# Kernel optimization log

Hardware: AMD Instinct MI355X
Metric: run time of the kernel (lower is better)

## Reference

```python
import jax, jax.numpy as jnp
import numpy as np
from jax import lax

VOCAB, NUM_CLASSES = 21128, 53
EMB, FILT, K = 128, 128, 3
B, L = 512, 512


def setup_inputs() -> dict:
    key = jax.random.key(0)
    ks = jax.random.split(key, 8)
    char_ids = jax.random.randint(ks[0], (B, L), 0, VOCAB, dtype=jnp.int64 if jax.config.jax_enable_x64 else jnp.int32)
    pos_e1 = jax.random.randint(ks[1], (B,), 0, L - 1, dtype=jnp.int32)
    pos_e2 = jax.random.randint(ks[2], (B,), 0, L - 1, dtype=jnp.int32)
    emb_table = jax.random.normal(ks[3], (VOCAB, EMB), dtype=jnp.float32) * 0.02
    emb_table = emb_table.at[0].set(0.0)  # padding_idx=0
    conv_w = jax.random.normal(ks[4], (FILT, EMB, K), dtype=jnp.float32) * (1.0 / np.sqrt(EMB * K))
    conv_b = jax.random.normal(ks[5], (FILT,), dtype=jnp.float32) * 0.01
    fc_w = jax.random.normal(ks[6], (NUM_CLASSES, FILT * 3), dtype=jnp.float32) * (1.0 / np.sqrt(FILT * 3))
    fc_b = jax.random.normal(ks[7], (NUM_CLASSES,), dtype=jnp.float32) * 0.01
    return {"char_ids": char_ids, "pos_e1": pos_e1, "pos_e2": pos_e2,
            "emb_table": emb_table, "conv_w": conv_w, "conv_b": conv_b,
            "fc_w": fc_w, "fc_b": fc_b}


def reference(char_ids, pos_e1, pos_e2, emb_table, conv_w, conv_b, fc_w, fc_b):
    b, seq = char_ids.shape
    x = emb_table[char_ids]                      # (b, L, E)
    x = jnp.transpose(x, (0, 2, 1))              # (b, E, L)
    conv_out = lax.conv_general_dilated(
        x, conv_w, window_strides=(1,), padding=[(K // 2, K // 2)],
        dimension_numbers=("NCH", "OIH", "NCH"))
    conv_out = jax.nn.relu(conv_out + conv_b[None, :, None])  # (b, F, L)

    # sort + clip entity boundaries, replicate e1==e2 -> e2=e1+1 adjustment
    e1 = jnp.clip(jnp.minimum(pos_e1, pos_e2), 0, seq)
    e2 = jnp.clip(jnp.maximum(pos_e1, pos_e2), 0, seq)
    e2 = jnp.where(e1 == e2, jnp.minimum(e1 + 1, seq), e2)

    idx = jnp.arange(seq)[None, :]               # (1, L)
    m1 = idx < jnp.maximum(e1, 1)[:, None]       # [:e1] or [:1] if e1==0
    m2 = (idx >= e1[:, None]) & (idx < e2[:, None])
    m3 = idx >= jnp.minimum(e2, seq - 1)[:, None]  # [e2:] or last col if e2==L

    neg = jnp.float32(-jnp.inf)
    def seg_max(mask):
        return jnp.max(jnp.where(mask[:, None, :], conv_out, neg), axis=-1)  # (b, F)

    pooled = jnp.concatenate([seg_max(m1), seg_max(m2), seg_max(m3)], axis=-1)  # (b, 3F)
    return pooled @ fc_w.T + fc_b
```

## Files before the change

kernel.cpp:

```cpp
#include <hip/hip_runtime.h>
#include <stdint.h>

#define VOCAB 21128
#define NUMC  53
#define EMB   128
#define SEQ   512
#define BATCH 512

typedef __bf16 bf16x8 __attribute__((ext_vector_type(8)));
typedef float f32x4 __attribute__((ext_vector_type(4)));

__device__ __forceinline__ unsigned int f2bf1(float f) {
    union { float f; unsigned int u; } v; v.f = f;
    return (v.u + 0x7FFFu + ((v.u >> 16) & 1u)) >> 16;
}
__device__ __forceinline__ unsigned int pack2(float a, float b) {
    return f2bf1(a) | (f2bf1(b) << 16);
}

__global__ void prep_kernel(const float* __restrict__ emb, const float* __restrict__ cw,
                            unsigned short* __restrict__ Tb, unsigned short* __restrict__ Wp) {
    int idx = blockIdx.x * blockDim.x + threadIdx.x;
    const int n8 = VOCAB * EMB / 8;
    if (idx < n8) {
        const float4* src = (const float4*)emb + (size_t)idx * 2;
        float4 a = src[0], b = src[1];
        uint4 o;
        o.x = pack2(a.x, a.y);
        o.y = pack2(a.z, a.w);
        o.z = pack2(b.x, b.y);
        o.w = pack2(b.z, b.w);
        *(uint4*)(Tb + (size_t)idx * 8) = o;
    }
    if (idx < 12 * 8 * 64 * 8) {
        int j = idx & 7, l = (idx >> 3) & 63, g = (idx >> 9) & 7, s = idx >> 12;
        int kk = s * 32 + (l >> 4) * 8 + j;
        int f = g * 16 + (l & 15);
        int tap = kk >> 7, e = kk & 127;
        Wp[idx] = (unsigned short)f2bf1(cw[(f * EMB + e) * 3 + tap]);
    }
}

__launch_bounds__(512, 2)
__global__ void pcnn_tile(const int* __restrict__ cid, const int* __restrict__ p1,
                          const int* __restrict__ p2,
                          const unsigned short* __restrict__ Tb,
                          const unsigned short* __restrict__ Wp,
                          float* __restrict__ Pd) {
    __shared__ __align__(16) unsigned short xs[130 * 136];
    __shared__ float pstage[2][3][128];

    const int bx   = blockIdx.x;
    const int b    = bx >> 2;
    const int tq   = bx & 3;
    const int tid  = threadIdx.x;
    const int lane = tid & 63;
    const int w    = tid >> 6;
    const int wm   = w & 1;
    const int wn   = w >> 1;
    const int quad = lane >> 4;
    const int lc   = lane & 15;

    const char* TbB = (const char*)Tb;
    const int cc = tid & 15;
    const int r0 = tid >> 4;
    int ids[5];
#pragma unroll
    for (int i = 0; i < 5; ++i) {
        int r = r0 + 32 * i;
        int p = tq * 128 + r - 1;
        ids[i] = (r < 130 && p >= 0 && p < SEQ) ? cid[(size_t)b * SEQ + p] : 0;
    }
    uint4 g[5];
#pragma unroll
    for (int i = 0; i < 5; ++i) {
        int r = r0 + 32 * i;
        if (r < 130) g[i] = *(const uint4*)(TbB + (size_t)(unsigned)ids[i] * 256u + cc * 16);
    }
#pragma unroll
    for (int i = 0; i < 5; ++i) {
        int r = r0 + 32 * i;
        if (r < 130) *(uint4*)(&xs[r * 136 + cc * 8]) = g[i];
    }

    int e1 = min(p1[b], p2[b]);
    int e2 = max(p1[b], p2[b]);
    if (e1 == e2) e2 = min(e1 + 1, SEQ);
    const int e1m = max(e1, 1);

    __syncthreads();

    f32x4 acc[4][2];
#pragma unroll
    for (int mt = 0; mt < 4; ++mt)
#pragma unroll
        for (int nt = 0; nt < 2; ++nt)
            acc[mt][nt] = (f32x4){0.f, 0.f, 0.f, 0.f};

#pragma unroll
    for (int s = 0; s < 12; ++s) {
        const int tap = s >> 2;
        const int eb  = (s & 3) * 32;
        bf16x8 b0 = *(const bf16x8*)(Wp + (size_t)((s * 8 + wn * 2) * 64 + lane) * 8);
        bf16x8 b1 = *(const bf16x8*)(Wp + (size_t)((s * 8 + wn * 2 + 1) * 64 + lane) * 8);
        bf16x8 af[4];
#pragma unroll
        for (int mt = 0; mt < 4; ++mt) {
            int r = wm * 64 + mt * 16 + lc + tap;
            af[mt] = *(const bf16x8*)(xs + r * 136 + eb + quad * 8);
        }
#pragma unroll
        for (int mt = 0; mt < 4; ++mt) {
            acc[mt][0] = __builtin_amdgcn_mfma_f32_16x16x32_bf16(af[mt], b0, acc[mt][0], 0, 0, 0);
            acc[mt][1] = __builtin_amdgcn_mfma_f32_16x16x32_bf16(af[mt], b1, acc[mt][1], 0, 0, 0);
        }
    }

    float smax[3][2];
#pragma unroll
    for (int s3 = 0; s3 < 3; ++s3) { smax[s3][0] = -1e30f; smax[s3][1] = -1e30f; }
#pragma unroll
    for (int mt = 0; mt < 4; ++mt)
#pragma unroll
        for (int reg = 0; reg < 4; ++reg) {
            int p = tq * 128 + wm * 64 + mt * 16 + quad * 4 + reg;
            float a0 = (p < e1m) ? 0.f : -2e30f;
            float a1 = (p >= e1 && p < e2) ? 0.f : -2e30f;
            float a2 = (p >= e2) ? 0.f : -2e30f;
#pragma unroll
            for (int nt = 0; nt < 2; ++nt) {
                float v = acc[mt][nt][reg];
                smax[0][nt] = fmaxf(smax[0][nt], v + a0);
                smax[1][nt] = fmaxf(smax[1][nt], v + a1);
                smax[2][nt] = fmaxf(smax[2][nt], v + a2);
            }
        }

#pragma unroll
    for (int s3 = 0; s3 < 3; ++s3)
#pragma unroll
        for (int nt = 0; nt < 2; ++nt) {
            float v = smax[s3][nt];
            v = fmaxf(v, __shfl_xor(v, 16));
            v = fmaxf(v, __shfl_xor(v, 32));
            smax[s3][nt] = v;
        }
    if (lane < 16) {
#pragma unroll
        for (int s3 = 0; s3 < 3; ++s3)
#pragma unroll
            for (int nt = 0; nt < 2; ++nt)
                pstage[wm][s3][(wn * 2 + nt) * 16 + lc] = smax[s3][nt];
    }
    __syncthreads();

    if (tid < 384) {
        int s3 = tid >> 7, f = tid & 127;
        Pd[((size_t)b * 4 + tq) * 384 + tid] = fmaxf(pstage[0][s3][f], pstage[1][s3][f]);
    }
}

__launch_bounds__(256, 4)
__global__ void pcnn_combine(const float* __restrict__ Pd, const float* __restrict__ cb,
                             const float* __restrict__ fcw, const float* __restrict__ fcb,
                             float* __restrict__ out) {
    __shared__ float pooled[384];
    __shared__ float fcred[NUMC][4];
    const int b = blockIdx.x;
    const int tid = threadIdx.x;

    for (int j = tid; j < 384; j += 256) {
        const float* pp = Pd + (size_t)b * 4 * 384 + j;
        float m = fmaxf(fmaxf(pp[0], pp[384]), fmaxf(pp[768], pp[1152]));
        pooled[j] = fmaxf(m + cb[j & 127], 0.f);
    }
    __syncthreads();

    if (tid < 212) {
        int c = tid >> 2, q = tid & 3;
        const float* wrow = fcw + (size_t)c * 384 + q * 96;
        const float* pp   = pooled + q * 96;
        float sum = 0.f;
#pragma unroll 8
        for (int i = 0; i < 96; ++i) sum += wrow[i] * pp[i];
        fcred[c][q] = sum;
    }
    __syncthreads();
    if (tid < NUMC)
        out[(size_t)b * NUMC + tid] =
            fcred[tid][0] + fcred[tid][1] + fcred[tid][2] + fcred[tid][3] + fcb[tid];
}

extern "C" void kernel_launch(void* const* d_in, const int* in_sizes, int n_in,
                              void* d_out, int out_size, void* d_ws, size_t ws_size,
                              hipStream_t stream) {
    const int*   cid = (const int*)d_in[0];
    const int*   p1  = (const int*)d_in[1];
    const int*   p2  = (const int*)d_in[2];
    const float* emb = (const float*)d_in[3];
    const float* cw  = (const float*)d_in[4];
    const float* cb  = (const float*)d_in[5];
    const float* fcw = (const float*)d_in[6];
    const float* fcb = (const float*)d_in[7];
    float* out = (float*)d_out;

    unsigned short* Tb = (unsigned short*)d_ws;
    unsigned short* Wp = (unsigned short*)((char*)d_ws + (size_t)VOCAB * EMB * 2);
    float*          Pd = (float*)((char*)d_ws + (size_t)VOCAB * EMB * 2 + 98304);

    const int n8 = VOCAB * EMB / 8;
    const int prep_threads = 256;
    const int prep_blocks  = (n8 + prep_threads - 1) / prep_threads;
    prep_kernel<<<prep_blocks, prep_threads, 0, stream>>>(emb, cw, Tb, Wp);
    pcnn_tile<<<BATCH * 4, 512, 0, stream>>>(cid, p1, p2, Tb, Wp, Pd);
    pcnn_combine<<<BATCH, 256, 0, stream>>>(Pd, cb, fcw, fcb, out);
}
```

Before: 130.7 us.

## Gather fp32 embeddings directly in tile kernel and shrink tiles to 64 rows

Drops the full-vocabulary bf16 conversion pass. The tile kernel now gathers fp32 embedding rows for its tokens and converts them to bf16 in registers while staging into LDS. The tile shrinks to 64 sequence positions with 128 threads (two waves, each covering 64 filters), and each wave writes its partial maxima straight to the workspace, removing the LDS staging and the second barrier. The combine kernel now reduces 8 partials per segment instead of 4. In exchange, gathers read twice as many bytes, halo rows are duplicated across more tiles, and each block issues fewer parallel loads.

```diff
diff --git a/kernel.cpp b/kernel.cpp
--- a/kernel.cpp
+++ b/kernel.cpp
@@ -18,20 +18,8 @@
     return f2bf1(a) | (f2bf1(b) << 16);
 }
 
-__global__ void prep_kernel(const float* __restrict__ emb, const float* __restrict__ cw,
-                            unsigned short* __restrict__ Tb, unsigned short* __restrict__ Wp) {
+__global__ void prep_w(const float* __restrict__ cw, unsigned short* __restrict__ Wp) {
     int idx = blockIdx.x * blockDim.x + threadIdx.x;
-    const int n8 = VOCAB * EMB / 8;
-    if (idx < n8) {
-        const float4* src = (const float4*)emb + (size_t)idx * 2;
-        float4 a = src[0], b = src[1];
-        uint4 o;
-        o.x = pack2(a.x, a.y);
-        o.y = pack2(a.z, a.w);
-        o.z = pack2(b.x, b.y);
-        o.w = pack2(b.z, b.w);
-        *(uint4*)(Tb + (size_t)idx * 8) = o;
-    }
     if (idx < 12 * 8 * 64 * 8) {
         int j = idx & 7, l = (idx >> 3) & 63, g = (idx >> 9) & 7, s = idx >> 12;
         int kk = s * 32 + (l >> 4) * 8 + j;
@@ -41,46 +29,38 @@
     }
 }
 
-__launch_bounds__(512, 2)
+__launch_bounds__(128)
 __global__ void pcnn_tile(const int* __restrict__ cid, const int* __restrict__ p1,
-                          const int* __restrict__ p2,
-                          const unsigned short* __restrict__ Tb,
+                          const int* __restrict__ p2, const float* __restrict__ emb,
                           const unsigned short* __restrict__ Wp,
                           float* __restrict__ Pd) {
-    __shared__ __align__(16) unsigned short xs[130 * 136];
-    __shared__ float pstage[2][3][128];
+    __shared__ __align__(16) unsigned short xs[66 * 136];
 
     const int bx   = blockIdx.x;
-    const int b    = bx >> 2;
-    const int tq   = bx & 3;
+    const int b    = bx >> 3;
+    const int tq   = bx & 7;
     const int tid  = threadIdx.x;
     const int lane = tid & 63;
-    const int w    = tid >> 6;
-    const int wm   = w & 1;
-    const int wn   = w >> 1;
+    const int wn   = tid >> 6;
     const int quad = lane >> 4;
     const int lc   = lane & 15;
 
-    const char* TbB = (const char*)Tb;
-    const int cc = tid & 15;
-    const int r0 = tid >> 4;
-    int ids[5];
 #pragma unroll
-    for (int i = 0; i < 5; ++i) {
-        int r = r0 + 32 * i;
-        int p = tq * 128 + r - 1;
-        ids[i] = (r < 130 && p >= 0 && p < SEQ) ? cid[(size_t)b * SEQ + p] : 0;
-    }
-    uint4 g[5];
-#pragma unroll
-    for (int i = 0; i < 5; ++i) {
-        int r = r0 + 32 * i;
-        if (r < 130) g[i] = *(const uint4*)(TbB + (size_t)(unsigned)ids[i] * 256u + cc * 16);
-    }
-#pragma unroll
-    for (int i = 0; i < 5; ++i) {
-        int r = r0 + 32 * i;
-        if (r < 130) *(uint4*)(&xs[r * 136 + cc * 8]) = g[i];
+    for (int i = 0; i < 9; ++i) {
+        int task = tid + 128 * i;
+        if (task < 1056) {
+            int r = task >> 4, c = task & 15;
+            int p = tq * 64 + r - 1;
+            int id = (p >= 0 && p < SEQ) ? cid[(size_t)b * SEQ + p] : 0;
+            const float4* src = (const float4*)(emb + (size_t)id * EMB + c * 8);
+            float4 a = src[0], d = src[1];
+            uint4 o;
+            o.x = pack2(a.x, a.y);
+            o.y = pack2(a.z, a.w);
+            o.z = pack2(d.x, d.y);
+            o.w = pack2(d.z, d.w);
+            *(uint4*)(&xs[r * 136 + c * 8]) = o;
+        }
     }
 
     int e1 = min(p1[b], p2[b]);
@@ -90,45 +70,49 @@
 
     __syncthreads();
 
-    f32x4 acc[4][2];
+    f32x4 acc[4][4];
 #pragma unroll
     for (int mt = 0; mt < 4; ++mt)
 #pragma unroll
-        for (int nt = 0; nt < 2; ++nt)
+        for (int nt = 0; nt < 4; ++nt)
             acc[mt][nt] = (f32x4){0.f, 0.f, 0.f, 0.f};
 
 #pragma unroll
     for (int s = 0; s < 12; ++s) {
         const int tap = s >> 2;
         const int eb  = (s & 3) * 32;
-        bf16x8 b0 = *(const bf16x8*)(Wp + (size_t)((s * 8 + wn * 2) * 64 + lane) * 8);
-        bf16x8 b1 = *(const bf16x8*)(Wp + (size_t)((s * 8 + wn * 2 + 1) * 64 + lane) * 8);
         bf16x8 af[4];
 #pragma unroll
         for (int mt = 0; mt < 4; ++mt) {
-            int r = wm * 64 + mt * 16 + lc + tap;
+            int r = mt * 16 + lc + tap;
             af[mt] = *(const bf16x8*)(xs + r * 136 + eb + quad * 8);
         }
 #pragma unroll
-        for (int mt = 0; mt < 4; ++mt) {
-            acc[mt][0] = __builtin_amdgcn_mfma_f32_16x16x32_bf16(af[mt], b0, acc[mt][0], 0, 0, 0);
-            acc[mt][1] = __builtin_amdgcn_mfma_f32_16x16x32_bf16(af[mt], b1, acc[mt][1], 0, 0, 0);
+        for (int nt = 0; nt < 4; ++nt) {
+            int g = wn * 4 + nt;
+            bf16x8 bf = *(const bf16x8*)(Wp + (size_t)((s * 8 + g) * 64 + lane) * 8);
+#pragma unroll
+            for (int mt = 0; mt < 4; ++mt)
+                acc[mt][nt] = __builtin_amdgcn_mfma_f32_16x16x32_bf16(af[mt], bf, acc[mt][nt], 0, 0, 0);
         }
     }
 
-    float smax[3][2];
+    float smax[3][4];
 #pragma unroll
-    for (int s3 = 0; s3 < 3; ++s3) { smax[s3][0] = -1e30f; smax[s3][1] = -1e30f; }
+    for (int s3 = 0; s3 < 3; ++s3)
+#pragma unroll
+        for (int nt = 0; nt < 4; ++nt) smax[s3][nt] = -1e30f;
+
 #pragma unroll
     for (int mt = 0; mt < 4; ++mt)
 #pragma unroll
         for (int reg = 0; reg < 4; ++reg) {
-            int p = tq * 128 + wm * 64 + mt * 16 + quad * 4 + reg;
+            int p = tq * 64 + mt * 16 + quad * 4 + reg;
             float a0 = (p < e1m) ? 0.f : -2e30f;
             float a1 = (p >= e1 && p < e2) ? 0.f : -2e30f;
             float a2 = (p >= e2) ? 0.f : -2e30f;
 #pragma unroll
-            for (int nt = 0; nt < 2; ++nt) {
+            for (int nt = 0; nt < 4; ++nt) {
                 float v = acc[mt][nt][reg];
                 smax[0][nt] = fmaxf(smax[0][nt], v + a0);
                 smax[1][nt] = fmaxf(smax[1][nt], v + a1);
@@ -139,24 +123,19 @@
 #pragma unroll
     for (int s3 = 0; s3 < 3; ++s3)
 #pragma unroll
-        for (int nt = 0; nt < 2; ++nt) {
+        for (int nt = 0; nt < 4; ++nt) {
             float v = smax[s3][nt];
             v = fmaxf(v, __shfl_xor(v, 16));
             v = fmaxf(v, __shfl_xor(v, 32));
             smax[s3][nt] = v;
         }
     if (lane < 16) {
+        size_t base = ((size_t)(b * 8 + tq) * 3) * 128;
 #pragma unroll
         for (int s3 = 0; s3 < 3; ++s3)
 #pragma unroll
-            for (int nt = 0; nt < 2; ++nt)
-                pstage[wm][s3][(wn * 2 + nt) * 16 + lc] = smax[s3][nt];
-    }
-    __syncthreads();
-
-    if (tid < 384) {
-        int s3 = tid >> 7, f = tid & 127;
-        Pd[((size_t)b * 4 + tq) * 384 + tid] = fmaxf(pstage[0][s3][f], pstage[1][s3][f]);
+            for (int nt = 0; nt < 4; ++nt)
+                Pd[base + (size_t)s3 * 128 + wn * 64 + nt * 16 + lc] = smax[s3][nt];
     }
 }
 
@@ -170,9 +149,12 @@
     const int tid = threadIdx.x;
 
     for (int j = tid; j < 384; j += 256) {
-        const float* pp = Pd + (size_t)b * 4 * 384 + j;
-        float m = fmaxf(fmaxf(pp[0], pp[384]), fmaxf(pp[768], pp[1152]));
-        pooled[j] = fmaxf(m + cb[j & 127], 0.f);
+        int s3 = j >> 7, f = j & 127;
+        const float* pp = Pd + ((size_t)b * 8 * 3 + s3) * 128 + f;
+        float m = -1e30f;
+#pragma unroll
+        for (int tq = 0; tq < 8; ++tq) m = fmaxf(m, pp[(size_t)tq * 384]);
+        pooled[j] = fmaxf(m + cb[f], 0.f);
     }
     __syncthreads();
 
@@ -204,14 +186,10 @@
     const float* fcb = (const float*)d_in[7];
     float* out = (float*)d_out;
 
-    unsigned short* Tb = (unsigned short*)d_ws;
-    unsigned short* Wp = (unsigned short*)((char*)d_ws + (size_t)VOCAB * EMB * 2);
-    float*          Pd = (float*)((char*)d_ws + (size_t)VOCAB * EMB * 2 + 98304);
+    unsigned short* Wp = (unsigned short*)d_ws;
+    float*          Pd = (float*)((char*)d_ws + 98304);
 
-    const int n8 = VOCAB * EMB / 8;
-    const int prep_threads = 256;
-    const int prep_blocks  = (n8 + prep_threads - 1) / prep_threads;
-    prep_kernel<<<prep_blocks, prep_threads, 0, stream>>>(emb, cw, Tb, Wp);
-    pcnn_tile<<<BATCH * 4, 512, 0, stream>>>(cid, p1, p2, Tb, Wp, Pd);
+    prep_w<<<96, 512, 0, stream>>>(cw, Wp);
+    pcnn_tile<<<BATCH * 8, 128, 0, stream>>>(cid, p1, p2, emb, Wp, Pd);
     pcnn_combine<<<BATCH, 256, 0, stream>>>(Pd, cb, fcw, fcb, out);
 }
```

After: 140.1 us. +7.2%, slower.

## Load embedding rows directly into MFMA fragments, drop LDS staging and sync

Applied to the files above, without the earlier changes.

The tile kernel no longer gathers embedding rows into shared memory. Each lane now computes row offsets for its three conv taps and loads A fragments straight from the bf16 table in global memory, which removes the LDS staging, both __syncthreads calls and the cross-wave pstage reduction. Tiles shrink to 64 positions with 4 waves, so the grid doubles to 8 tiles per batch row and the combine kernel reduces over 8 partials. In exchange, every embedding row is fetched from global or L2 three times (once per tap) and through strided 16-byte loads, and the partial-output buffer doubles in size.

```diff
diff --git a/kernel.cpp b/kernel.cpp
--- a/kernel.cpp
+++ b/kernel.cpp
@@ -41,54 +41,38 @@
     }
 }
 
-__launch_bounds__(512, 2)
+__launch_bounds__(256)
 __global__ void pcnn_tile(const int* __restrict__ cid, const int* __restrict__ p1,
                           const int* __restrict__ p2,
                           const unsigned short* __restrict__ Tb,
                           const unsigned short* __restrict__ Wp,
                           float* __restrict__ Pd) {
-    __shared__ __align__(16) unsigned short xs[130 * 136];
-    __shared__ float pstage[2][3][128];
-
     const int bx   = blockIdx.x;
-    const int b    = bx >> 2;
-    const int tq   = bx & 3;
+    const int b    = bx >> 3;
+    const int tq   = bx & 7;
     const int tid  = threadIdx.x;
     const int lane = tid & 63;
-    const int w    = tid >> 6;
-    const int wm   = w & 1;
-    const int wn   = w >> 1;
+    const int wn   = tid >> 6;
     const int quad = lane >> 4;
     const int lc   = lane & 15;
 
+    const int* crow = cid + (size_t)b * SEQ;
     const char* TbB = (const char*)Tb;
-    const int cc = tid & 15;
-    const int r0 = tid >> 4;
-    int ids[5];
+
+    unsigned int roff[4][3];
 #pragma unroll
-    for (int i = 0; i < 5; ++i) {
-        int r = r0 + 32 * i;
-        int p = tq * 128 + r - 1;
-        ids[i] = (r < 130 && p >= 0 && p < SEQ) ? cid[(size_t)b * SEQ + p] : 0;
-    }
-    uint4 g[5];
+    for (int mt = 0; mt < 4; ++mt)
 #pragma unroll
-    for (int i = 0; i < 5; ++i) {
-        int r = r0 + 32 * i;
-        if (r < 130) g[i] = *(const uint4*)(TbB + (size_t)(unsigned)ids[i] * 256u + cc * 16);
-    }
-#pragma unroll
-    for (int i = 0; i < 5; ++i) {
-        int r = r0 + 32 * i;
-        if (r < 130) *(uint4*)(&xs[r * 136 + cc * 8]) = g[i];
-    }
+        for (int tap = 0; tap < 3; ++tap) {
+            int p = tq * 64 + mt * 16 + lc + tap - 1;
+            unsigned int id = (p >= 0 && p < SEQ) ? (unsigned int)crow[p] : 0u;
+            roff[mt][tap] = id * 256u;
+        }
 
     int e1 = min(p1[b], p2[b]);
     int e2 = max(p1[b], p2[b]);
     if (e1 == e2) e2 = min(e1 + 1, SEQ);
     const int e1m = max(e1, 1);
-
-    __syncthreads();
 
     f32x4 acc[4][2];
 #pragma unroll
@@ -99,16 +83,14 @@
 
 #pragma unroll
     for (int s = 0; s < 12; ++s) {
-        const int tap = s >> 2;
-        const int eb  = (s & 3) * 32;
+        const int tap  = s >> 2;
+        const int coff = (s & 3) * 64 + quad * 16;
+        bf16x8 af[4];
+#pragma unroll
+        for (int mt = 0; mt < 4; ++mt)
+            af[mt] = *(const bf16x8*)(TbB + roff[mt][tap] + coff);
         bf16x8 b0 = *(const bf16x8*)(Wp + (size_t)((s * 8 + wn * 2) * 64 + lane) * 8);
         bf16x8 b1 = *(const bf16x8*)(Wp + (size_t)((s * 8 + wn * 2 + 1) * 64 + lane) * 8);
-        bf16x8 af[4];
-#pragma unroll
-        for (int mt = 0; mt < 4; ++mt) {
-            int r = wm * 64 + mt * 16 + lc + tap;
-            af[mt] = *(const bf16x8*)(xs + r * 136 + eb + quad * 8);
-        }
 #pragma unroll
         for (int mt = 0; mt < 4; ++mt) {
             acc[mt][0] = __builtin_amdgcn_mfma_f32_16x16x32_bf16(af[mt], b0, acc[mt][0], 0, 0, 0);
@@ -119,11 +101,12 @@
     float smax[3][2];
 #pragma unroll
     for (int s3 = 0; s3 < 3; ++s3) { smax[s3][0] = -1e30f; smax[s3][1] = -1e30f; }
+
 #pragma unroll
     for (int mt = 0; mt < 4; ++mt)
 #pragma unroll
         for (int reg = 0; reg < 4; ++reg) {
-            int p = tq * 128 + wm * 64 + mt * 16 + quad * 4 + reg;
+            int p = tq * 64 + mt * 16 + quad * 4 + reg;
             float a0 = (p < e1m) ? 0.f : -2e30f;
             float a1 = (p >= e1 && p < e2) ? 0.f : -2e30f;
             float a2 = (p >= e2) ? 0.f : -2e30f;
@@ -146,17 +129,12 @@
             smax[s3][nt] = v;
         }
     if (lane < 16) {
+        size_t base = ((size_t)(b * 8 + tq) * 3) * 128;
 #pragma unroll
         for (int s3 = 0; s3 < 3; ++s3)
 #pragma unroll
             for (int nt = 0; nt < 2; ++nt)
-                pstage[wm][s3][(wn * 2 + nt) * 16 + lc] = smax[s3][nt];
-    }
-    __syncthreads();
-
-    if (tid < 384) {
-        int s3 = tid >> 7, f = tid & 127;
-        Pd[((size_t)b * 4 + tq) * 384 + tid] = fmaxf(pstage[0][s3][f], pstage[1][s3][f]);
+                Pd[base + (size_t)s3 * 128 + (wn * 2 + nt) * 16 + lc] = smax[s3][nt];
     }
 }
 
@@ -170,9 +148,12 @@
     const int tid = threadIdx.x;
 
     for (int j = tid; j < 384; j += 256) {
-        const float* pp = Pd + (size_t)b * 4 * 384 + j;
-        float m = fmaxf(fmaxf(pp[0], pp[384]), fmaxf(pp[768], pp[1152]));
-        pooled[j] = fmaxf(m + cb[j & 127], 0.f);
+        int s3 = j >> 7, f = j & 127;
+        const float* pp = Pd + ((size_t)b * 8 * 3 + s3) * 128 + f;
+        float m = -1e30f;
+#pragma unroll
+        for (int tq = 0; tq < 8; ++tq) m = fmaxf(m, pp[(size_t)tq * 384]);
+        pooled[j] = fmaxf(m + cb[f], 0.f);
     }
     __syncthreads();
 
@@ -212,6 +193,6 @@
     const int prep_threads = 256;
     const int prep_blocks  = (n8 + prep_threads - 1) / prep_threads;
     prep_kernel<<<prep_blocks, prep_threads, 0, stream>>>(emb, cw, Tb, Wp);
-    pcnn_tile<<<BATCH * 4, 512, 0, stream>>>(cid, p1, p2, Tb, Wp, Pd);
+    pcnn_tile<<<BATCH * 8, 256, 0, stream>>>(cid, p1, p2, Tb, Wp, Pd);
     pcnn_combine<<<BATCH, 256, 0, stream>>>(Pd, cb, fcw, fcb, out);
 }
```

New measurement: 186.8 us. 42.9% more time.
